# Kernel optimization log

Hardware: AMD Instinct MI355X
Metric: run time of the kernel (lower is better)

The kernel has to match this reference:

```python
import jax, jax.numpy as jnp
import numpy as np

B, T, I, H = 64, 512, 1024, 1024  # batch, seq_len, input_size, hidden_size


def setup_inputs() -> dict:
    key = jax.random.key(0)
    ks = jax.random.split(key, 5)
    s = 0.02
    return {
        "sequence": jax.random.normal(ks[0], (B, T, I), jnp.float32),
        "Wx0": jax.random.normal(ks[1], (4 * H, I), jnp.float32) * s,
        "Wh0": jax.random.normal(ks[2], (4 * H, H), jnp.float32) * s,
        "b0": jnp.zeros((4 * H,), jnp.float32),
        "Wx1": jax.random.normal(ks[3], (4 * H, H), jnp.float32) * s,
        "Wh1": jax.random.normal(ks[4], (4 * H, H), jnp.float32) * s,
        "b1": jnp.zeros((4 * H,), jnp.float32),
    }


def _run_layer(xs, Wx, Wh, b):
    # xs: [T, B, D_in]; packed gates order: forget, input-gate(w), candidate(i), output(m)
    batch = xs.shape[1]
    hid = Wh.shape[1]
    # precompute input projections for all timesteps: [T, B, 4H]
    xproj = jnp.einsum('tbd,gd->tbg', xs, Wx) + b

    def step(carry, xp):
        c, h = carry
        z = xp + h @ Wh.T  # [B, 4H]
        f, w, i, m = jnp.split(z, 4, axis=-1)
        c = c * jax.nn.sigmoid(f) + jax.nn.sigmoid(w) * jnp.tanh(i)
        h = jnp.tanh(c) * jax.nn.sigmoid(m)
        return (c, h), h

    init = (jnp.zeros((batch, hid), xs.dtype), jnp.zeros((batch, hid), xs.dtype))
    (c, h), hs = jax.lax.scan(step, init, xproj)
    return hs, h  # hs: [T, B, H], h: [B, H]


def reference(sequence, Wx0, Wh0, b0, Wx1, Wh1, b1):
    xs = jnp.transpose(sequence, (1, 0, 2))  # [T, B, I]
    hs0, _ = _run_layer(xs, Wx0, Wh0, b0)
    _, h_last = _run_layer(hs0, Wx1, Wh1, b1)
    return h_last  # [B, H] == H[:, :, -1] of the original
```

## Files before the change

kernel.cpp:

```cpp
#include <hip/hip_runtime.h>

typedef __bf16 bf16x8 __attribute__((ext_vector_type(8)));
typedef float f32x4 __attribute__((ext_vector_type(4)));
typedef unsigned long long u64;

__device__ inline float sigm(float x) { return 1.0f / (1.0f + __expf(-x)); }
__device__ inline float tanh_f(float x) {
    float e = __expf(2.0f * x);
    return 1.0f - 2.0f / (e + 1.0f);
}

__device__ inline unsigned short f2bf(float f) {
    __bf16 h = (__bf16)f;
    return __builtin_bit_cast(unsigned short, h);
}

__device__ inline bf16x8 cvt8(float4 lo, float4 hi) {
    bf16x8 r;
    r[0] = (__bf16)lo.x; r[1] = (__bf16)lo.y; r[2] = (__bf16)lo.z; r[3] = (__bf16)lo.w;
    r[4] = (__bf16)hi.x; r[5] = (__bf16)hi.y; r[6] = (__bf16)hi.z; r[7] = (__bf16)hi.w;
    return r;
}

__device__ inline u64 ld64c(const u64* p) {
    return __hip_atomic_load(p, __ATOMIC_RELAXED, __HIP_MEMORY_SCOPE_AGENT);
}
__device__ inline void st32c(unsigned int* p, unsigned int v) {
    __hip_atomic_store(p, v, __ATOMIC_RELAXED, __HIP_MEMORY_SCOPE_AGENT);
}
__device__ inline unsigned int ld32c(const unsigned int* p) {
    return __hip_atomic_load(p, __ATOMIC_RELAXED, __HIP_MEMORY_SCOPE_AGENT);
}
__device__ inline void st16c(unsigned short* p, unsigned short v) {
    __hip_atomic_store(p, v, __ATOMIC_RELAXED, __HIP_MEMORY_SCOPE_AGENT);
}


__global__ void cvt_weights(const float* __restrict__ Wx0, const float* __restrict__ Wh0,
                            const float* __restrict__ Wx1, const float* __restrict__ Wh1,
                            unsigned short* __restrict__ W0, unsigned short* __restrict__ W1) {
    size_t idx = ((size_t)blockIdx.x * 256 + threadIdx.x) * 8;
    const size_t LSZ = (size_t)4096 * 2048;
    int layer = idx >= LSZ;
    size_t e = idx - (layer ? LSZ : 0);
    int row = (int)(e >> 11);
    int k = (int)(e & 2047);
    const float* src = layer ? (k < 1024 ? Wx1 : Wh1) : (k < 1024 ? Wx0 : Wh0);
    const float* s = src + (size_t)row * 1024 + (k & 1023);
    float4 lo = ((const float4*)s)[0], hi = ((const float4*)s)[1];
    *reinterpret_cast<bf16x8*>((layer ? W1 : W0) + e) = cvt8(lo, hi);
}

__global__ void cvt_seq(const float* __restrict__ seq, unsigned short* __restrict__ seqb, int T) {
    int t = blockIdx.x >> 6, b = blockIdx.x & 63;
    int row = b & 31, btile = b >> 5, tid = threadIdx.x;
    const float* s = seq + ((size_t)b * T + t) * 1024 + tid * 8;
    float4 lo = ((const float4*)s)[0], hi = ((const float4*)s)[1];
    int off = ((row >> 4) << 14) + ((tid >> 2) << 9) + (((tid & 3) << 4) + (row & 15)) * 8;
    *reinterpret_cast<bf16x8*>(seqb + ((size_t)t * 2 + btile) * 32768 + off) = cvt8(lo, hi);
}

struct Smem {
    unsigned short ah[32768];
    unsigned short ax[32768];
    float zh[4][32][16];
    float zx[2][4][32][16];
};

struct StageRegs { u64 q[32]; };

__device__ inline void stage_issue(StageRegs& r, const unsigned short* __restrict__ src, int ttid) {
#pragma unroll
    for (int i = 0; i < 16; ++i) {
        const u64* s = (const u64*)(src + (size_t)((ttid + (i << 8)) << 3));
        r.q[2 * i] = ld64c(s);
        r.q[2 * i + 1] = ld64c(s + 1);
    }
}
__device__ inline void stage_issue_plain(StageRegs& r, const unsigned short* __restrict__ src, int ttid) {
#pragma unroll
    for (int i = 0; i < 16; ++i) {
        const u64* s = (const u64*)(src + (size_t)((ttid + (i << 8)) << 3));
        r.q[2 * i] = s[0];
        r.q[2 * i + 1] = s[1];
    }
}
__device__ inline void stage_write(const StageRegs& r, unsigned short* tile, int ttid) {
#pragma unroll
    for (int i = 0; i < 16; ++i) {
        u64* d = (u64*)(tile + (size_t)((ttid + (i << 8)) << 3));
        d[0] = r.q[2 * i];
        d[1] = r.q[2 * i + 1];
    }
}

template <bool SEQB>
__global__ __launch_bounds__(512, 2) void lstm_persistent(
    const float* __restrict__ seq, const unsigned short* __restrict__ seqb,
    const unsigned short* __restrict__ W0, const unsigned short* __restrict__ W1,
    const float* __restrict__ bias0, const float* __restrict__ bias1,
    unsigned short* h0buf, unsigned short* h1buf, unsigned int* flags,
    float* out, int T) {
    const int bid = blockIdx.x;
    const int r = bid & 7, q = bid >> 3;
    const int btile = q & 1, t2 = q >> 1;
    const int layer = t2 >> 3;
    const int jtile = ((t2 & 7) << 3) | r;
    const int j0 = jtile * 16;
    const int brow = btile * 32;

    const int tid = threadIdx.x;
    const int isX = tid >> 8;
    const int ttid = tid & 255;
    const int twave = ttid >> 6;
    const int lane = tid & 63;
    const int ln15 = lane & 15, lhi = lane >> 4;

    const unsigned short* Wl = layer ? W1 : W0;
    const float* bias = layer ? bias1 : bias0;
    unsigned short* hown = layer ? h1buf : h0buf;

    __shared__ Smem sm;
    unsigned short* mytile = isX ? sm.ax : sm.ah;

    const unsigned short* Bb =
        Wl + (size_t)(twave * 1024 + j0 + ln15) * 2048 + (isX ? 0 : 1024) + lhi * 8;
    bf16x8 wreg[32];
#pragma unroll
    for (int k = 0; k < 32; ++k) wreg[k] = *(const bf16x8*)(Bb + k * 32);

    const int bl = tid >> 4;
    const int jj = tid & 15;
    const int colg = j0 + jj;
    const float b_f = bias[colg], b_w = bias[1024 + colg];
    const float b_i = bias[2048 + colg], b_m = bias[3072 + colg];
    const int hoff = ((bl >> 4) << 14) + ((colg >> 5) << 9) +
                     ((((colg >> 3) & 3) << 4) + (bl & 15)) * 8 + (colg & 7);
    float creg = 0.f;

    const int P = T + 3;
    for (int p = 0; p < P; ++p) {
        const int tx = layer ? (p - 2) : p;
        const int th = layer ? (p - 3) : (p - 1);
        const bool actx = (tx >= 0) && (tx < T);
        const bool acth = (th >= 0) && (th < T);
        const bool myact = isX ? actx : acth;

        if (p > 0 && myact && !(isX && layer == 0)) {
            const unsigned int tgt = (unsigned int)p;
            const unsigned int* f = &flags[(isX ? 0 : layer * 128) + (tid & 127)];
            while (ld32c(f) < tgt) __builtin_amdgcn_s_sleep(1);
        }

        if (myact) {
            StageRegs s;
            if (isX) {
                if (layer == 0) {
                    if (SEQB) {
                        stage_issue_plain(s, seqb + ((size_t)tx * 2 + btile) * 32768, ttid);
                        stage_write(s, sm.ax, ttid);
                    }
                } else {
                    stage_issue(s, h0buf + (size_t)((tx & 1) * 2 + btile) * 32768, ttid);
                    stage_write(s, sm.ax, ttid);
                }
            } else {
                stage_issue(s, hown + (size_t)(((th - 1) & 1) * 2 + btile) * 32768, ttid);
                stage_write(s, sm.ah, ttid);
            }
        }
        __syncthreads();

        if (myact) {
            f32x4 acc0 = {0.f, 0.f, 0.f, 0.f};
            f32x4 acc1 = {0.f, 0.f, 0.f, 0.f};
            if (isX && layer == 0 && !SEQB) {
                const float* a0f = seq + ((size_t)(brow + ln15) * T + tx) * 1024 + lhi * 8;
                const float* a1f = a0f + (size_t)16 * T * 1024;
#pragma unroll
                for (int kk = 0; kk < 32; ++kk) {
                    float4 l0 = ((const float4*)a0f)[0], h0v = ((const float4*)a0f)[1];
                    float4 l1 = ((const float4*)a1f)[0], h1v = ((const float4*)a1f)[1];
                    bf16x8 av0 = cvt8(l0, h0v), av1 = cvt8(l1, h1v);
                    acc0 = __builtin_amdgcn_mfma_f32_16x16x32_bf16(av0, wreg[kk], acc0, 0, 0, 0);
                    acc1 = __builtin_amdgcn_mfma_f32_16x16x32_bf16(av1, wreg[kk], acc1, 0, 0, 0);
                    a0f += 32; a1f += 32;
                }
            } else {
                const unsigned short* tile = mytile;
                if (!isX) __builtin_amdgcn_s_setprio(1);
#pragma unroll
                for (int kk = 0; kk < 32; ++kk) {
                    bf16x8 av0 = *(const bf16x8*)(tile + kk * 512 + lane * 8);
                    bf16x8 av1 = *(const bf16x8*)(tile + 16384 + kk * 512 + lane * 8);
                    acc0 = __builtin_amdgcn_mfma_f32_16x16x32_bf16(av0, wreg[kk], acc0, 0, 0, 0);
                    acc1 = __builtin_amdgcn_mfma_f32_16x16x32_bf16(av1, wreg[kk], acc1, 0, 0, 0);
                }
                if (!isX) __builtin_amdgcn_s_setprio(0);
            }
            float* zd = isX ? &sm.zx[tx & 1][twave][0][0] : &sm.zh[twave][0][0];
#pragma unroll
            for (int rr = 0; rr < 4; ++rr) {
                zd[(4 * lhi + rr) * 16 + ln15] = acc0[rr];
                zd[(16 + 4 * lhi + rr) * 16 + ln15] = acc1[rr];
            }
        }
        __syncthreads();

        if (acth) {
            const int zb = th & 1;
            float zf = sm.zh[0][bl][jj] + sm.zx[zb][0][bl][jj] + b_f;
            float zw = sm.zh[1][bl][jj] + sm.zx[zb][1][bl][jj] + b_w;
            float zi = sm.zh[2][bl][jj] + sm.zx[zb][2][bl][jj] + b_i;
            float zm = sm.zh[3][bl][jj] + sm.zx[zb][3][bl][jj] + b_m;
            float cn = creg * sigm(zf) + sigm(zw) * tanh_f(zi);
            float h = tanh_f(cn) * sigm(zm);
            creg = cn;
            unsigned short* tb = hown + (size_t)((th & 1) * 2 + btile) * 32768;
            st16c(tb + hoff, f2bf(h));
            if (layer && th == T - 1) out[(brow + bl) * 1024 + colg] = h;
        }

        if (p < P - 1) {
            __syncthreads();
            if (tid == 0) st32c(&flags[bid], (unsigned int)(p + 1));
        }
    }
}

extern "C" void kernel_launch(void* const* d_in, const int* in_sizes, int n_in,
                              void* d_out, int out_size, void* d_ws, size_t ws_size,
                              hipStream_t stream) {
    const float* seq = (const float*)d_in[0];
    const float* Wx0 = (const float*)d_in[1];
    const float* Wh0 = (const float*)d_in[2];
    const float* b0 = (const float*)d_in[3];
    const float* Wx1 = (const float*)d_in[4];
    const float* Wh1 = (const float*)d_in[5];
    const float* b1 = (const float*)d_in[6];
    float* out = (float*)d_out;
    char* ws = (char*)d_ws;
    const int T = 512;

    const size_t WBYTES = (size_t)4096 * 2048 * 2;
    const size_t SEQB_BYTES = (size_t)512 * 2 * 32768 * 2;
    const size_t H0_BYTES = 2 * 2 * 65536;
    const size_t H1_BYTES = 2 * 2 * 65536;
    const size_t STATE_BYTES = H0_BYTES + H1_BYTES + 1024;

    size_t offSeqb = 2 * WBYTES;
    bool big = ws_size >= 2 * WBYTES + SEQB_BYTES + STATE_BYTES;
    size_t offState = big ? (offSeqb + SEQB_BYTES) : offSeqb;

    unsigned short* W0p = (unsigned short*)(ws);
    unsigned short* W1p = (unsigned short*)(ws + WBYTES);
    unsigned short* seqbp = (unsigned short*)(ws + offSeqb);
    unsigned short* h0p = (unsigned short*)(ws + offState);
    unsigned short* h1p = (unsigned short*)(ws + offState + H0_BYTES);
    unsigned int* flagsp = (unsigned int*)(ws + offState + H0_BYTES + H1_BYTES);

    hipLaunchKernelGGL(cvt_weights, dim3(8192), dim3(256), 0, stream,
                       Wx0, Wh0, Wx1, Wh1, W0p, W1p);
    if (big)
        hipLaunchKernelGGL(cvt_seq, dim3(T * 64), dim3(128), 0, stream, seq, seqbp, T);
    hipMemsetAsync(ws + offState, 0, STATE_BYTES, stream);

    int Tv = T;
    void* args[] = {&seq, &seqbp, &W0p, &W1p, &b0, &b1, &h0p, &h1p, &flagsp, &out, &Tv};
    if (big) {
        hipError_t e = hipLaunchCooperativeKernel((void*)lstm_persistent<true>,
                                                  dim3(256), dim3(512), args, 0, stream);
        if (e != hipSuccess) {
            hipLaunchKernelGGL((lstm_persistent<true>), dim3(256), dim3(512), 0, stream,
                               seq, seqbp, W0p, W1p, b0, b1, h0p, h1p, flagsp, out, Tv);
        }
    } else {
        hipError_t e = hipLaunchCooperativeKernel((void*)lstm_persistent<false>,
                                                  dim3(256), dim3(512), args, 0, stream);
        if (e != hipSuccess) {
            hipLaunchKernelGGL((lstm_persistent<false>), dim3(256), dim3(512), 0, stream,
                               seq, seqbp, W0p, W1p, b0, b1, h0p, h1p, flagsp, out, Tv);
        }
    }
}
```

Measured before the change: 3.744 ms.

## Prefetch x-tile before flag wait and triple-buffer layer-0 hidden state

The x-input stage load is now issued before the spin-wait on inter-block flags, so its global latency overlaps the barrier wait. Every thread now waits on all 256 flags in a single uniform barrier, replacing per-role partial waits. Layer 0's hidden buffer becomes three-deep and layer 1 lags by one more step, so layer 1's reads of h0 do not race with layer 0 overwriting the slot. The cost is an extra pipeline step, a stricter global wait for all blocks, and an extra syncthreads per step.

```diff
diff --git a/kernel.cpp b/kernel.cpp
--- a/kernel.cpp
+++ b/kernel.cpp
@@ -121,7 +121,6 @@
     unsigned short* hown = layer ? h1buf : h0buf;
 
     __shared__ Smem sm;
-    unsigned short* mytile = isX ? sm.ax : sm.ah;
 
     const unsigned short* Bb =
         Wl + (size_t)(twave * 1024 + j0 + ln15) * 2048 + (isX ? 0 : 1024) + lhi * 8;
@@ -138,39 +137,42 @@
                      ((((colg >> 3) & 3) << 4) + (bl & 15)) * 8 + (colg & 7);
     float creg = 0.f;
 
-    const int P = T + 3;
+    const int P = T + 4;
     for (int p = 0; p < P; ++p) {
-        const int tx = layer ? (p - 2) : p;
-        const int th = layer ? (p - 3) : (p - 1);
+        const int tx = layer ? (p - 3) : p;
+        const int th = layer ? (p - 4) : (p - 1);
         const bool actx = (tx >= 0) && (tx < T);
         const bool acth = (th >= 0) && (th < T);
-        const bool myact = isX ? actx : acth;
-
-        if (p > 0 && myact && !(isX && layer == 0)) {
-            const unsigned int tgt = (unsigned int)p;
-            const unsigned int* f = &flags[(isX ? 0 : layer * 128) + (tid & 127)];
-            while (ld32c(f) < tgt) __builtin_amdgcn_s_sleep(1);
-        }
-
-        if (myact) {
-            StageRegs s;
-            if (isX) {
-                if (layer == 0) {
-                    if (SEQB) {
-                        stage_issue_plain(s, seqb + ((size_t)tx * 2 + btile) * 32768, ttid);
-                        stage_write(s, sm.ax, ttid);
-                    }
-                } else {
-                    stage_issue(s, h0buf + (size_t)((tx & 1) * 2 + btile) * 32768, ttid);
-                    stage_write(s, sm.ax, ttid);
+
+        StageRegs sx;
+        bool havex = false;
+        if (isX && actx) {
+            if (layer == 0) {
+                if (SEQB) {
+                    stage_issue_plain(sx, seqb + ((size_t)tx * 2 + btile) * 32768, ttid);
+                    havex = true;
                 }
             } else {
-                stage_issue(s, hown + (size_t)(((th - 1) & 1) * 2 + btile) * 32768, ttid);
-                stage_write(s, sm.ah, ttid);
+                stage_issue(sx, h0buf + (size_t)((tx % 3) * 2 + btile) * 32768, ttid);
+                havex = true;
             }
         }
+
+        if (p > 0) {
+            while (ld32c(&flags[ttid]) < (unsigned int)p) __builtin_amdgcn_s_sleep(1);
+        }
         __syncthreads();
 
+        if (havex) stage_write(sx, sm.ax, ttid);
+        if (!isX && acth) {
+            StageRegs sh;
+            const int hslot = layer ? ((th + 1) & 1) : ((th + 2) % 3);
+            stage_issue(sh, hown + (size_t)(hslot * 2 + btile) * 32768, ttid);
+            stage_write(sh, sm.ah, ttid);
+        }
+        __syncthreads();
+
+        const bool myact = isX ? actx : acth;
         if (myact) {
             f32x4 acc0 = {0.f, 0.f, 0.f, 0.f};
             f32x4 acc1 = {0.f, 0.f, 0.f, 0.f};
@@ -187,7 +189,7 @@
                     a0f += 32; a1f += 32;
                 }
             } else {
-                const unsigned short* tile = mytile;
+                const unsigned short* tile = isX ? sm.ax : sm.ah;
                 if (!isX) __builtin_amdgcn_s_setprio(1);
 #pragma unroll
                 for (int kk = 0; kk < 32; ++kk) {
@@ -216,7 +218,8 @@
             float cn = creg * sigm(zf) + sigm(zw) * tanh_f(zi);
             float h = tanh_f(cn) * sigm(zm);
             creg = cn;
-            unsigned short* tb = hown + (size_t)((th & 1) * 2 + btile) * 32768;
+            const int wbuf = layer ? (th & 1) : (th % 3);
+            unsigned short* tb = hown + (size_t)(wbuf * 2 + btile) * 32768;
             st16c(tb + hoff, f2bf(h));
             if (layer && th == T - 1) out[(brow + bl) * 1024 + colg] = h;
         }
@@ -244,7 +247,7 @@
 
     const size_t WBYTES = (size_t)4096 * 2048 * 2;
     const size_t SEQB_BYTES = (size_t)512 * 2 * 32768 * 2;
-    const size_t H0_BYTES = 2 * 2 * 65536;
+    const size_t H0_BYTES = 3 * 2 * 65536;
     const size_t H1_BYTES = 2 * 2 * 65536;
     const size_t STATE_BYTES = H0_BYTES + H1_BYTES + 1024;
 
```

New measurement: 5.101 ms. 1.36x slower.
